# Kernel tuning notes

Hardware: AMD Instinct MI355X
Metric: run time of the kernel (lower is better)

## Reference

```python
import jax, jax.numpy as jnp
import numpy as np


def setup_inputs() -> dict:
    key = jax.random.key(0)
    k1, k2, k3 = jax.random.split(key, 3)
    bs, n1, n2, d1, d2, dout = 4, 128, 128, 768, 768, 768
    input1 = jax.random.normal(k1, (bs, n1, d1), dtype=jnp.float32)
    input2 = jax.random.normal(k2, (bs, n2, d2), dtype=jnp.float32)
    # torch Linear(sum_dims, dout): we store W as (d1+d2, dout) so y = x @ W + b
    W = jax.random.normal(k3, (d1 + d2, dout), dtype=jnp.float32) * (1.0 / np.sqrt(d1 + d2))
    b = jnp.zeros((dout,), dtype=jnp.float32)
    return {"input1": input1, "input2": input2, "W": W, "b": b}


def reference(input1, input2, W, b):
    # Original: expand to [bs,n1,n2,d1]/[bs,n1,n2,d2], cat -> [bs,n1,n2,d1+d2], Linear.
    # Algebraically identical without materializing the concat:
    #   cat([x1,x2]) @ W = x1 @ W[:d1] + x2 @ W[d1:]
    d1 = input1.shape[-1]
    W1, W2 = W[:d1], W[d1:]
    p1 = jnp.einsum("bnd,do->bno", input1, W1)  # [bs, n1, dout]
    p2 = jnp.einsum("bmd,do->bmo", input2, W2)  # [bs, n2, dout]
    # broadcast-sum over the pair grid -> [bs, n1, n2, dout]
    return p1[:, :, None, :] + p2[:, None, :, :] + b
```

## Files before the change

kernel.cpp:

```cpp
#include <hip/hip_runtime.h>

typedef float f4    __attribute__((ext_vector_type(4)));
typedef float f32x4 __attribute__((ext_vector_type(4)));
typedef short short8 __attribute__((ext_vector_type(8)));
typedef unsigned short u16;
typedef unsigned short u16x4 __attribute__((ext_vector_type(4)));

#define NCHUNK 24

#define AWS_U16 1572864u
#define WWS_U16 2359296u

__device__ inline u16 f2bf(float x) {
    union { float f; unsigned u; } v; v.f = x;
    return (u16)((v.u + 0x7FFFu + ((v.u >> 16) & 1u)) >> 16);
}
__device__ inline float bf2f(u16 h) {
    union { unsigned u; float f; } v; v.u = ((unsigned)h) << 16;
    return v.f;
}

__global__ __launch_bounds__(512) void convert_kernel(
    const float* __restrict__ A1, const float* __restrict__ A2,
    const float* __restrict__ W, u16* __restrict__ Aws, u16* __restrict__ Wws)
{
    const int id = blockIdx.x * 512 + threadIdx.x;
    if (blockIdx.x < 384) {
        const int u   = id;
        const int row = u / 192;
        const int k   = (u - row * 192) * 4;
        const float* src = (row < 512) ? (A1 + (size_t)row * 768 + k)
                                       : (A2 + (size_t)(row - 512) * 768 + k);
        const f4 v = *(const f4*)src;
        u16x4 h, l;
        #pragma unroll
        for (int j = 0; j < 4; ++j) { h[j] = f2bf(v[j]); l[j] = f2bf(v[j] - bf2f(h[j])); }
        const int g = row >> 6, rt = (row >> 4) & 3, r = row & 15;
        const int c = k >> 5, kq = (k >> 3) & 3, ki0 = k & 7;
        const size_t base = (size_t)g * 98304 + c * 4096 + rt * 512 + kq * 128 + r * 8 + ki0;
        *(u16x4*)&Aws[base]        = h;
        *(u16x4*)&Aws[base + 2048] = l;
    } else {
        const int u   = id - 384 * 512;
        const int o   = u % 768;
        const int kk4 = u / 768;
        const int kk  = kk4 * 4;
        const int z   = (kk4 >= 192);
        const int k   = kk - z * 768;
        u16x4 h, l;
        #pragma unroll
        for (int j = 0; j < 4; ++j) {
            const float v = W[(size_t)(kk + j) * 768 + o];
            h[j] = f2bf(v); l[j] = f2bf(v - bf2f(h[j]));
        }
        const int rt = o >> 4, r = o & 15;
        const int c = k >> 5, kq = (k >> 3) & 3, ki0 = k & 7;
        const size_t base = (size_t)c * 98304 + (size_t)z * 49152
                          + rt * 512 + kq * 128 + r * 8 + ki0;
        *(u16x4*)&Wws[base]         = h;
        *(u16x4*)&Wws[base + 24576] = l;
    }
}

__global__ __launch_bounds__(512) void mfma_direct_kernel(
    const u16* __restrict__ Aws, const u16* __restrict__ Wws,
    const float* __restrict__ bias, float* __restrict__ out)
{
    __shared__ float p[128][68];

    const int o0 = blockIdx.x * 64;
    const int nm = blockIdx.y;
    const int b  = nm >> 2, hn = (nm >> 1) & 1, hm = nm & 1;
    const int n0 = hn * 64, m0 = hm * 64;
    const int g_n = b * 2 + hn;
    const int g_m = 8 + b * 2 + hm;
    const int t = threadIdx.x, lane = t & 63, w = t >> 6;
    const int rt0 = blockIdx.x * 4;

    const u16* aBase = Aws + (size_t)((w < 4) ? g_n : g_m) * 98304
                     + (w & 3) * 512 + lane * 8;
    const u16* bBase = Wws + (size_t)((w < 4) ? 0 : 1) * 49152
                     + rt0 * 512 + lane * 8;

    f32x4 acc[4] = {0, 0, 0, 0};

    #pragma unroll 2
    for (int c = 0; c < NCHUNK; ++c) {
        const u16* ap = aBase + (size_t)c * 4096;
        const u16* bp = bBase + (size_t)c * 98304;
        const short8 ah = *(const short8*)(ap);
        const short8 al = *(const short8*)(ap + 2048);
        #pragma unroll
        for (int ct = 0; ct < 4; ++ct) {
            const short8 bh = *(const short8*)(bp + ct * 512);
            const short8 bl = *(const short8*)(bp + 24576 + ct * 512);
            acc[ct] = __builtin_amdgcn_mfma_f32_16x16x32_bf16(ah, bh, acc[ct], 0, 0, 0);
            acc[ct] = __builtin_amdgcn_mfma_f32_16x16x32_bf16(ah, bl, acc[ct], 0, 0, 0);
            acc[ct] = __builtin_amdgcn_mfma_f32_16x16x32_bf16(al, bh, acc[ct], 0, 0, 0);
        }
    }

    #pragma unroll
    for (int ct = 0; ct < 4; ++ct)
        #pragma unroll
        for (int i = 0; i < 4; ++i)
            p[w * 16 + (lane >> 4) * 4 + i][ct * 16 + (lane & 15)] = acc[ct][i];
    __syncthreads();

    const int o4 = (t & 15) * 4;
    const int nn = t >> 4;
    const f4 bb  = *(const f4*)(bias + o0 + o4);
    const f4 p1a = *(const f4*)&p[nn * 2 + 0][o4] + bb;
    const f4 p1b = *(const f4*)&p[nn * 2 + 1][o4] + bb;

    float* ob = out + ((size_t)(b * 128 + n0 + nn * 2) * 128 + m0) * 768 + o0 + o4;
    const size_t nstride = (size_t)128 * 768;

    #pragma unroll 4
    for (int m = 0; m < 64; ++m) {
        const f4 p2v = *(const f4*)&p[64 + m][o4];
        __builtin_nontemporal_store(p1a + p2v, (f4*)(ob + (size_t)m * 768));
        __builtin_nontemporal_store(p1b + p2v, (f4*)(ob + nstride + (size_t)m * 768));
    }
}

__global__ __launch_bounds__(512) void fused_v6(
    const float* __restrict__ A1, const float* __restrict__ A2,
    const float* __restrict__ W, const float* __restrict__ bias,
    float* __restrict__ out)
{
    __shared__ union {
        struct { u16 Ah[4096], Al[4096], Bh[4096], Bl[4096]; } s;
        float p[128][68];
    } u;

    const int o0 = blockIdx.x * 64;
    const int nm = blockIdx.y;
    const int b  = nm >> 2;
    const int n0 = ((nm >> 1) & 1) * 64;
    const int m0 = (nm & 1) * 64;
    const int t = threadIdx.x, lane = t & 63, w = t >> 6;

    const float* aptr[2]; int a_dst[2];
    #pragma unroll
    for (int q = 0; q < 2; ++q) {
        const int a = t + q * 512, rc = a >> 3, k0 = (a & 7) * 4;
        const float* base = (rc < 64) ? (A1 + (size_t)(b * 128 + n0 + rc) * 768)
                                      : (A2 + (size_t)(b * 128 + m0 + (rc - 64)) * 768);
        aptr[q] = base + k0;
        a_dst[q] = (rc >> 4) * 512 + (k0 >> 3) * 128 + (rc & 15) * 8 + (k0 & 7);
    }
    const float* bptr[2]; int b_dst[2];
    #pragma unroll
    for (int q = 0; q < 2; ++q) {
        const int v = t + q * 512, oc = v & 127, kk = (v >> 7) * 4, z = oc >> 6;
        bptr[q] = W + (size_t)(z * 768 + kk) * 768 + (o0 + (oc & 63));
        b_dst[q] = (oc >> 4) * 512 + (kk >> 3) * 128 + (oc & 15) * 8 + (kk & 7);
    }

    f4 rA[2]; float rB[2][4];
    #pragma unroll
    for (int q = 0; q < 2; ++q) {
        rA[q] = *(const f4*)(aptr[q]);
        #pragma unroll
        for (int j = 0; j < 4; ++j) rB[q][j] = bptr[q][(size_t)j * 768];
    }

    f32x4 acc[4] = {0, 0, 0, 0};
    for (int c = 0; c < NCHUNK; ++c) {
        #pragma unroll
        for (int q = 0; q < 2; ++q) {
            u16x4 h, l;
            #pragma unroll
            for (int j = 0; j < 4; ++j) { h[j] = f2bf(rA[q][j]); l[j] = f2bf(rA[q][j] - bf2f(h[j])); }
            *(u16x4*)&u.s.Ah[a_dst[q]] = h; *(u16x4*)&u.s.Al[a_dst[q]] = l;
        }
        #pragma unroll
        for (int q = 0; q < 2; ++q) {
            u16x4 h, l;
            #pragma unroll
            for (int j = 0; j < 4; ++j) { h[j] = f2bf(rB[q][j]); l[j] = f2bf(rB[q][j] - bf2f(h[j])); }
            *(u16x4*)&u.s.Bh[b_dst[q]] = h; *(u16x4*)&u.s.Bl[b_dst[q]] = l;
        }
        __syncthreads();
        if (c + 1 < NCHUNK) {
            const int k0 = (c + 1) * 32;
            #pragma unroll
            for (int q = 0; q < 2; ++q) {
                rA[q] = *(const f4*)(aptr[q] + k0);
                #pragma unroll
                for (int j = 0; j < 4; ++j) rB[q][j] = bptr[q][(size_t)(k0 + j) * 768];
            }
        }
        {
            const short8 ah = *(const short8*)&u.s.Ah[w * 512 + lane * 8];
            const short8 al = *(const short8*)&u.s.Al[w * 512 + lane * 8];
            const int bt0 = (w >> 2) * 4;
            #pragma unroll
            for (int ct = 0; ct < 4; ++ct) {
                const short8 bh = *(const short8*)&u.s.Bh[(bt0 + ct) * 512 + lane * 8];
                const short8 bl = *(const short8*)&u.s.Bl[(bt0 + ct) * 512 + lane * 8];
                acc[ct] = __builtin_amdgcn_mfma_f32_16x16x32_bf16(ah, bh, acc[ct], 0, 0, 0);
                acc[ct] = __builtin_amdgcn_mfma_f32_16x16x32_bf16(ah, bl, acc[ct], 0, 0, 0);
                acc[ct] = __builtin_amdgcn_mfma_f32_16x16x32_bf16(al, bh, acc[ct], 0, 0, 0);
            }
        }
        __syncthreads();
    }
    #pragma unroll
    for (int ct = 0; ct < 4; ++ct)
        #pragma unroll
        for (int i = 0; i < 4; ++i)
            u.p[w * 16 + (lane >> 4) * 4 + i][ct * 16 + (lane & 15)] = acc[ct][i];
    __syncthreads();

    const int o4 = (t & 15) * 4, nn = t >> 4;
    const f4 bb  = *(const f4*)(bias + o0 + o4);
    const f4 p1a = *(const f4*)&u.p[nn * 2 + 0][o4] + bb;
    const f4 p1b = *(const f4*)&u.p[nn * 2 + 1][o4] + bb;
    float* ob = out + ((size_t)(b * 128 + n0 + nn * 2) * 128 + m0) * 768 + o0 + o4;
    const size_t nstride = (size_t)128 * 768;
    #pragma unroll 4
    for (int m = 0; m < 64; ++m) {
        const f4 p2v = *(const f4*)&u.p[64 + m][o4];
        __builtin_nontemporal_store(p1a + p2v, (f4*)(ob + (size_t)m * 768));
        __builtin_nontemporal_store(p1b + p2v, (f4*)(ob + nstride + (size_t)m * 768));
    }
}

extern "C" void kernel_launch(void* const* d_in, const int* in_sizes, int n_in,
                              void* d_out, int out_size, void* d_ws, size_t ws_size,
                              hipStream_t stream)
{
    const float* input1 = (const float*)d_in[0];
    const float* input2 = (const float*)d_in[1];
    const float* W      = (const float*)d_in[2];
    const float* bias   = (const float*)d_in[3];
    float* out = (float*)d_out;

    const size_t need = (size_t)(AWS_U16 + WWS_U16) * sizeof(u16);

    if (ws_size >= need) {
        u16* Aws = (u16*)d_ws;
        u16* Wws = Aws + AWS_U16;
        convert_kernel<<<dim3(960), 512, 0, stream>>>(input1, input2, W, Aws, Wws);
        mfma_direct_kernel<<<dim3(12, 16), 512, 0, stream>>>(Aws, Wws, bias, out);
    } else {
        fused_v6<<<dim3(12, 16), 512, 0, stream>>>(input1, input2, W, bias, out);
    }
}
```

Baseline: 245.9 us.

## Split GEMM and broadcast-add into separate kernels via workspace projections

The GEMM kernel now computes each projection row block exactly once and writes p1 and p2 (with bias folded into p2) to a workspace buffer. Before, each 64x64 tile block recomputed both projections. A new broadcast kernel then reads these projections and streams the pair-grid sum to the output with 2048 blocks, which should give better store parallelism than 192 blocks. The cost is an extra kernel launch and a round trip of the projections through global memory.

```diff
diff --git a/kernel.cpp b/kernel.cpp
--- a/kernel.cpp
+++ b/kernel.cpp
@@ -10,6 +10,7 @@
 
 #define AWS_U16 1572864u
 #define WWS_U16 2359296u
+#define P_FLOATS ((size_t)1024 * 768)
 
 __device__ inline u16 f2bf(float x) {
     union { float f; unsigned u; } v; v.f = x;
@@ -62,22 +63,16 @@
     }
 }
 
-__global__ __launch_bounds__(512) void mfma_direct_kernel(
+__global__ __launch_bounds__(512) void mfma_p_kernel(
     const u16* __restrict__ Aws, const u16* __restrict__ Wws,
-    const float* __restrict__ bias, float* __restrict__ out)
-{
-    __shared__ float p[128][68];
-
+    const float* __restrict__ bias, float* __restrict__ P)
+{
     const int o0 = blockIdx.x * 64;
-    const int nm = blockIdx.y;
-    const int b  = nm >> 2, hn = (nm >> 1) & 1, hm = nm & 1;
-    const int n0 = hn * 64, m0 = hm * 64;
-    const int g_n = b * 2 + hn;
-    const int g_m = 8 + b * 2 + hm;
+    const int z  = blockIdx.y;
     const int t = threadIdx.x, lane = t & 63, w = t >> 6;
     const int rt0 = blockIdx.x * 4;
 
-    const u16* aBase = Aws + (size_t)((w < 4) ? g_n : g_m) * 98304
+    const u16* aBase = Aws + (size_t)((w < 4) ? z : 8 + z) * 98304
                      + (w & 3) * 512 + lane * 8;
     const u16* bBase = Wws + (size_t)((w < 4) ? 0 : 1) * 49152
                      + rt0 * 512 + lane * 8;
@@ -100,27 +95,41 @@
         }
     }
 
+    const int col = o0 + (lane & 15);
+    if (w >= 4) {
+        #pragma unroll
+        for (int ct = 0; ct < 4; ++ct) {
+            const float bv = bias[col + ct * 16];
+            #pragma unroll
+            for (int i = 0; i < 4; ++i) acc[ct][i] += bv;
+        }
+    }
+
+    const int row0 = ((w < 4) ? z * 64 : 512 + z * 64) + (w & 3) * 16 + (lane >> 4) * 4;
     #pragma unroll
     for (int ct = 0; ct < 4; ++ct)
         #pragma unroll
         for (int i = 0; i < 4; ++i)
-            p[w * 16 + (lane >> 4) * 4 + i][ct * 16 + (lane & 15)] = acc[ct][i];
-    __syncthreads();
-
-    const int o4 = (t & 15) * 4;
-    const int nn = t >> 4;
-    const f4 bb  = *(const f4*)(bias + o0 + o4);
-    const f4 p1a = *(const f4*)&p[nn * 2 + 0][o4] + bb;
-    const f4 p1b = *(const f4*)&p[nn * 2 + 1][o4] + bb;
-
-    float* ob = out + ((size_t)(b * 128 + n0 + nn * 2) * 128 + m0) * 768 + o0 + o4;
-    const size_t nstride = (size_t)128 * 768;
+            P[(size_t)(row0 + i) * 768 + col + ct * 16] = acc[ct][i];
+}
+
+__global__ __launch_bounds__(192) void bcast_kernel(
+    const float* __restrict__ P, float* __restrict__ out)
+{
+    const int t     = threadIdx.x;
+    const int bn    = blockIdx.x;
+    const int b     = bn >> 7;
+    const int mbase = blockIdx.y * 32;
+
+    const f4 p1v = *(const f4*)(P + (size_t)bn * 768 + t * 4);
+    const float* p2base = P + (size_t)(512 + b * 128) * 768 + t * 4;
+    float* obase = out + (size_t)bn * (128 * 768) + t * 4;
 
     #pragma unroll 4
-    for (int m = 0; m < 64; ++m) {
-        const f4 p2v = *(const f4*)&p[64 + m][o4];
-        __builtin_nontemporal_store(p1a + p2v, (f4*)(ob + (size_t)m * 768));
-        __builtin_nontemporal_store(p1b + p2v, (f4*)(ob + nstride + (size_t)m * 768));
+    for (int mm = 0; mm < 32; ++mm) {
+        const int m = mbase + mm;
+        const f4 v = p1v + *(const f4*)(p2base + (size_t)m * 768);
+        __builtin_nontemporal_store(v, (f4*)(obase + (size_t)m * 768));
     }
 }
 
@@ -238,13 +247,16 @@
     const float* bias   = (const float*)d_in[3];
     float* out = (float*)d_out;
 
-    const size_t need = (size_t)(AWS_U16 + WWS_U16) * sizeof(u16);
+    const size_t need = (size_t)(AWS_U16 + WWS_U16) * sizeof(u16)
+                      + P_FLOATS * sizeof(float);
 
     if (ws_size >= need) {
         u16* Aws = (u16*)d_ws;
         u16* Wws = Aws + AWS_U16;
+        float* P = (float*)(Wws + WWS_U16);
         convert_kernel<<<dim3(960), 512, 0, stream>>>(input1, input2, W, Aws, Wws);
-        mfma_direct_kernel<<<dim3(12, 16), 512, 0, stream>>>(Aws, Wws, bias, out);
+        mfma_p_kernel<<<dim3(12, 8), 512, 0, stream>>>(Aws, Wws, bias, P);
+        bcast_kernel<<<dim3(512, 4), 192, 0, stream>>>(P, out);
     } else {
         fused_v6<<<dim3(12, 16), 512, 0, stream>>>(input1, input2, W, bias, out);
     }
```

Result: no change. 245.4 us (-0.2%).
